# Kernel optimization log

Hardware: AMD Instinct MI355X
Metric: run time of the kernel (lower is better)

The kernel has to match this reference:

```python
import jax, jax.numpy as jnp
import numpy as np
import math

SEQLEN, DIM, N_HEADS = 2048, 4096, 32
HEAD_DIM = DIM // N_HEADS
NEG_INF = -1e30  # exp underflows to exactly 0, same effect as -inf without NaN risk


def setup_inputs() -> dict:
    key = jax.random.key(0)
    ks = jax.random.split(key, 7)
    scale = 1.0 / math.sqrt(DIM)
    x = jax.random.normal(ks[0], (SEQLEN, DIM), dtype=jnp.float32)
    weight_q = jax.random.normal(ks[1], (DIM, DIM), dtype=jnp.float32) * scale
    weight_k = jax.random.normal(ks[2], (DIM, DIM), dtype=jnp.float32) * scale
    weight_v = jax.random.normal(ks[3], (DIM, DIM), dtype=jnp.float32) * scale
    weight_o = jax.random.normal(ks[4], (DIM, DIM), dtype=jnp.float32) * scale
    # RoPE frequencies: freqs_cis = exp(i * t * theta_j), standard LLaMA schedule
    inv_freq = 1.0 / (10000.0 ** (np.arange(0, HEAD_DIM, 2, dtype=np.float32) / HEAD_DIM))
    angles = np.arange(SEQLEN, dtype=np.float32)[:, None] * inv_freq[None, :]  # [S, hd/2]
    freqs_cos = jnp.asarray(np.cos(angles), dtype=jnp.float32)
    freqs_sin = jnp.asarray(np.sin(angles), dtype=jnp.float32)
    # additive causal mask [S, S]
    mask = jnp.where(jnp.triu(jnp.ones((SEQLEN, SEQLEN), dtype=bool), k=1), NEG_INF, 0.0).astype(jnp.float32)
    return {"x": x, "weight_q": weight_q, "weight_k": weight_k, "weight_v": weight_v,
            "weight_o": weight_o, "freqs_cos": freqs_cos, "freqs_sin": freqs_sin,
            "mask": mask, "start_pos": 0}


def _apply_rope(t, cos, sin):
    # t: [S, H, hd]; cos/sin: [S, hd/2]
    tr = t.reshape(*t.shape[:-1], -1, 2)           # [S, H, hd/2, 2]
    t_re, t_im = tr[..., 0], tr[..., 1]
    c = cos[:, None, :]
    s = sin[:, None, :]
    out_re = t_re * c - t_im * s
    out_im = t_re * s + t_im * c
    return jnp.stack([out_re, out_im], axis=-1).reshape(t.shape)


def reference(x, weight_q, weight_k, weight_v, weight_o, freqs_cos, freqs_sin, mask, start_pos):
    S, D = x.shape
    hd = freqs_cos.shape[-1] * 2
    H = D // hd
    # the per-head double loop over wq[j][i] is exactly a full [D,D] projection
    xq = (x @ weight_q).reshape(S, H, hd)
    xk = (x @ weight_k).reshape(S, H, hd)
    xv = (x @ weight_v).reshape(S, H, hd)
    xq = _apply_rope(xq, freqs_cos, freqs_sin)
    xk = _apply_rope(xk, freqs_cos, freqs_sin)
    # start_pos == 0 prefill: cache slice == freshly computed keys/values
    scores = jnp.einsum('shd,thd->hst', xq, xk) / jnp.sqrt(jnp.float32(hd))
    scores = scores + mask[None, :, :]
    probs = jax.nn.softmax(scores.astype(jnp.float32), axis=-1).astype(xq.dtype)
    qkv = jnp.einsum('hst,thd->shd', probs, xv).reshape(S, D)
    return qkv @ weight_o
```

## Files before the change

### kernel.cpp

```cpp
#include <hip/hip_runtime.h>
#include <hip/hip_bf16.h>
#include <type_traits>

typedef __hip_bfloat16 bf16;
typedef __attribute__((ext_vector_type(8))) short s8v;
typedef __attribute__((ext_vector_type(4))) short s4v;
typedef __attribute__((ext_vector_type(4))) float f4v;

#define MFMA16(A, B, C) __builtin_amdgcn_mfma_f32_16x16x32_bf16((A), (B), (C), 0, 0, 0)

constexpr int SEQ = 2048;
constexpr int DIM = 4096;
constexpr int NH  = 32;
constexpr int HD  = 128;

__device__ __forceinline__ short f2bs(float f) {
    __hip_bfloat16_raw r = __float2bfloat16(f);
    return (short)r.x;
}

__device__ __forceinline__ void ld_g2l(const bf16* g, bf16* l) {
    __builtin_amdgcn_global_load_lds(
        (const __attribute__((address_space(1))) void*)g,
        (__attribute__((address_space(3))) void*)l, 16, 0, 0);
}

__global__ void convert_bf16(const float* __restrict__ s, bf16* __restrict__ d) {
    int i = blockIdx.x * blockDim.x + threadIdx.x;
    float4 f = ((const float4*)s)[i];
    s4v o;
    o[0] = f2bs(f.x); o[1] = f2bs(f.y); o[2] = f2bs(f.z); o[3] = f2bs(f.w);
    *(s4v*)(d + (size_t)i * 4) = o;
}

__global__ void convt_bf16(const float* __restrict__ src, bf16* __restrict__ dst,
                           int R, int C) {
    __shared__ float t[32][33];
    int c0 = blockIdx.x * 32, r0 = blockIdx.y * 32;
    int tx = threadIdx.x, ty = threadIdx.y;
#pragma unroll
    for (int i = 0; i < 4; i++)
        t[ty + 8 * i][tx] = src[(size_t)(r0 + ty + 8 * i) * C + c0 + tx];
    __syncthreads();
#pragma unroll
    for (int i = 0; i < 4; i++)
        dst[(size_t)(c0 + ty + 8 * i) * R + r0 + tx] = __float2bfloat16(t[tx][ty + 8 * i]);
}

template <typename CT>
__global__ __launch_bounds__(512, 2) void gemm_8p(const bf16* __restrict__ A,
                                                  const bf16* __restrict__ Bt,
                                                  CT* __restrict__ C,
                                                  int M, int N, int K) {
    __shared__ bf16 As_[2][128 * 64];
    __shared__ bf16 Bs_[2][256 * 64];
    const int tid  = threadIdx.x;
    const int lane = tid & 63;
    const int wv   = tid >> 6;
    const int m16  = lane & 15;
    const int quad = lane >> 4;
    const int wm   = wv >> 2, wn = wv & 3;
    const int bm   = blockIdx.y, bn = blockIdx.x;

    const bf16* Ab = A  + (size_t)bm * 128 * K;
    const bf16* Bb = Bt + (size_t)bn * 256 * K;

    const int i0   = wv * 64 + lane;
    const int row0 = i0 >> 3;
    const int gc8  = ((i0 & 7) ^ (row0 & 7)) * 8;
    const int dst0 = (wv * 64) * 8;
    const int dst1 = (512 + wv * 64) * 8;

    const int aB = (wm * 64 + m16) * 64;
    const int bB = (wn * 64 + m16) * 64;
    const int swz = m16 & 7;
    const int c0k = ((0 + quad) ^ swz) * 8;
    const int c1k = ((4 + quad) ^ swz) * 8;

    const int NT = K >> 6;

    f4v acc[4][4] = {};
    s8v aR[4][2], bR[4][2];

#define STAGEU(gb, lb) do { \
        ld_g2l((gb) + (size_t)row0 * K + gc8, (lb) + dst0); \
        ld_g2l((gb) + (size_t)(row0 + 64) * K + gc8, (lb) + dst1); } while (0)
#define LDA_(i, ks) aR[i][ks] = *(const s8v*)(Ac + aB + (i) * 1024 + ((ks) ? c1k : c0k))
#define LDB_(j, ks) bR[j][ks] = *(const s8v*)(Bc + bB + (j) * 1024 + ((ks) ? c1k : c0k))
#define MMQ(i, j) do { acc[i][j] = MFMA16(aR[i][0], bR[j][0], acc[i][j]); \
                       acc[i][j] = MFMA16(aR[i][1], bR[j][1], acc[i][j]); } while (0)
#define BARX()  __builtin_amdgcn_s_barrier()
#define LGKM0() do { asm volatile("s_waitcnt lgkmcnt(0)" ::: "memory"); \
                     __builtin_amdgcn_sched_barrier(0); } while (0)

    STAGEU(Ab, As_[0]);
    STAGEU(Bb, Bs_[0]);
    STAGEU(Bb + (size_t)128 * K, Bs_[0] + 128 * 64);
    if (NT > 1) {
        STAGEU(Bb + 64, Bs_[1]);
        STAGEU(Bb + (size_t)128 * K + 64, Bs_[1] + 128 * 64);
        STAGEU(Ab + 64, As_[1]);
        asm volatile("s_waitcnt vmcnt(6)" ::: "memory");
    } else {
        asm volatile("s_waitcnt vmcnt(0)" ::: "memory");
    }
    __builtin_amdgcn_sched_barrier(0);
    BARX();

    for (int t = 0; t < NT; ++t) {
        const int cur = t & 1;
        const bf16* Ac = As_[cur];
        const bf16* Bc = Bs_[cur];
        const bool more = (t + 2 < NT);
        const int k2 = (t + 2) << 6;

        LDA_(0, 0); LDA_(0, 1); LDA_(1, 0); LDA_(1, 1);
        LDB_(0, 0); LDB_(0, 1); LDB_(1, 0); LDB_(1, 1);
        BARX(); LGKM0();
        __builtin_amdgcn_s_setprio(1);
        MMQ(0, 0); MMQ(0, 1); MMQ(1, 0); MMQ(1, 1);
        __builtin_amdgcn_s_setprio(0);
        BARX();

        LDB_(2, 0); LDB_(2, 1); LDB_(3, 0); LDB_(3, 1);
        BARX(); LGKM0();
        __builtin_amdgcn_s_setprio(1);
        MMQ(0, 2); MMQ(0, 3); MMQ(1, 2); MMQ(1, 3);
        __builtin_amdgcn_s_setprio(0);
        BARX();

        LDA_(2, 0); LDA_(2, 1); LDA_(3, 0); LDA_(3, 1);
        if (more) {
            STAGEU(Bb + k2, Bs_[cur]);
            STAGEU(Bb + (size_t)128 * K + k2, Bs_[cur] + 128 * 64);
        }
        BARX(); LGKM0();
        __builtin_amdgcn_s_setprio(1);
        MMQ(2, 0); MMQ(2, 1); MMQ(3, 0); MMQ(3, 1);
        __builtin_amdgcn_s_setprio(0);
        BARX();

        if (more) {
            STAGEU(Ab + k2, As_[cur]);
            asm volatile("s_waitcnt vmcnt(6)" ::: "memory");
        } else {
            asm volatile("s_waitcnt vmcnt(0)" ::: "memory");
        }
        __builtin_amdgcn_sched_barrier(0);
        BARX();
        __builtin_amdgcn_s_setprio(1);
        MMQ(2, 2); MMQ(2, 3); MMQ(3, 2); MMQ(3, 3);
        __builtin_amdgcn_s_setprio(0);
        BARX();
    }

#undef STAGEU
#undef LDA_
#undef LDB_
#undef MMQ
#undef BARX
#undef LGKM0

#pragma unroll
    for (int i = 0; i < 4; i++)
#pragma unroll
        for (int j = 0; j < 4; j++)
#pragma unroll
            for (int r = 0; r < 4; r++) {
                int row = bm * 128 + wm * 64 + i * 16 + quad * 4 + r;
                int col = bn * 256 + wn * 64 + j * 16 + m16;
                if constexpr (std::is_same<CT, float>::value)
                    C[(size_t)row * N + col] = acc[i][j][r];
                else
                    C[(size_t)row * N + col] = __float2bfloat16(acc[i][j][r]);
            }
}

template <typename AT, typename CT>
__global__ __launch_bounds__(256) void gemm_nat(const AT* __restrict__ A,
                                                const float* __restrict__ B,
                                                CT* __restrict__ C,
                                                int M, int N, int K) {
    __shared__ short As[128][40];
    __shared__ short Bs[128][40];
    const int tid  = threadIdx.x;
    const int lane = tid & 63;
    const int w    = tid >> 6;
    const int m16  = lane & 15;
    const int quad = lane >> 4;
    const int wm   = w >> 1, wn = w & 1;
    const int bm   = blockIdx.y, bn = blockIdx.x;

    const AT* Ab = A + (size_t)bm * 128 * K;

    f4v acc[4][4] = {};
    const int r0 = tid >> 2;
    const int kc = (tid & 3) * 8;

    for (int k0 = 0; k0 < K; k0 += 32) {
        if constexpr (std::is_same<AT, float>::value) {
#pragma unroll
            for (int half = 0; half < 2; half++) {
                const float* src = Ab + (size_t)(r0 + 64 * half) * K + k0 + kc;
                float4 f0 = *(const float4*)(src);
                float4 f1 = *(const float4*)(src + 4);
                s8v t;
                t[0] = f2bs(f0.x); t[1] = f2bs(f0.y); t[2] = f2bs(f0.z); t[3] = f2bs(f0.w);
                t[4] = f2bs(f1.x); t[5] = f2bs(f1.y); t[6] = f2bs(f1.z); t[7] = f2bs(f1.w);
                *(s8v*)&As[r0 + 64 * half][kc] = t;
            }
        } else {
            *(s8v*)&As[r0][kc]      = *(const s8v*)(Ab + (size_t)r0 * K + k0 + kc);
            *(s8v*)&As[r0 + 64][kc] = *(const s8v*)(Ab + (size_t)(r0 + 64) * K + k0 + kc);
        }
#pragma unroll
        for (int v = tid; v < 512; v += 256) {
            int kr = v >> 4;
            int nc = (v & 15) * 8;
            const float* src = B + (size_t)(k0 + kr) * N + bn * 128 + nc;
            float4 f0 = *(const float4*)(src);
            float4 f1 = *(const float4*)(src + 4);
            Bs[nc + 0][kr] = f2bs(f0.x); Bs[nc + 1][kr] = f2bs(f0.y);
            Bs[nc + 2][kr] = f2bs(f0.z); Bs[nc + 3][kr] = f2bs(f0.w);
            Bs[nc + 4][kr] = f2bs(f1.x); Bs[nc + 5][kr] = f2bs(f1.y);
            Bs[nc + 6][kr] = f2bs(f1.z); Bs[nc + 7][kr] = f2bs(f1.w);
        }
        __syncthreads();

        s8v a[4], b[4];
#pragma unroll
        for (int i = 0; i < 4; i++) a[i] = *(s8v*)&As[wm * 64 + i * 16 + m16][quad * 8];
#pragma unroll
        for (int j = 0; j < 4; j++) b[j] = *(s8v*)&Bs[wn * 64 + j * 16 + m16][quad * 8];
#pragma unroll
        for (int i = 0; i < 4; i++)
#pragma unroll
            for (int j = 0; j < 4; j++) acc[i][j] = MFMA16(a[i], b[j], acc[i][j]);
        __syncthreads();
    }

#pragma unroll
    for (int i = 0; i < 4; i++)
#pragma unroll
        for (int j = 0; j < 4; j++)
#pragma unroll
            for (int r = 0; r < 4; r++) {
                int row = bm * 128 + wm * 64 + i * 16 + quad * 4 + r;
                int col = bn * 128 + wn * 64 + j * 16 + m16;
                if constexpr (std::is_same<CT, float>::value)
                    C[(size_t)row * N + col] = acc[i][j][r];
                else
                    C[(size_t)row * N + col] = __float2bfloat16(acc[i][j][r]);
            }
}

__global__ void rope_kernel(bf16* __restrict__ Q, bf16* __restrict__ K,
                            const float* __restrict__ fc, const float* __restrict__ fs) {
    int tid = blockIdx.x * blockDim.x + threadIdx.x;
    int s = tid >> 11;
    int r = tid & 2047;
    int i = r & 63;
    float c  = fc[s * 64 + i];
    float sn = fs[s * 64 + i];
    size_t idx = (size_t)s * DIM + 2 * r;
    float qre = __bfloat162float(Q[idx]), qim = __bfloat162float(Q[idx + 1]);
    Q[idx]     = __float2bfloat16(qre * c - qim * sn);
    Q[idx + 1] = __float2bfloat16(qre * sn + qim * c);
    float kre = __bfloat162float(K[idx]), kim = __bfloat162float(K[idx + 1]);
    K[idx]     = __float2bfloat16(kre * c - kim * sn);
    K[idx + 1] = __float2bfloat16(kre * sn + kim * c);
}

__global__ __launch_bounds__(256) void attn_kernel(const bf16* __restrict__ Q,
                                                   const bf16* __restrict__ K,
                                                   const bf16* __restrict__ V,
                                                   bf16* __restrict__ O) {
    __shared__ short Ks[64][136];
    __shared__ short Vs[128][72];
    __shared__ short Ps[64][72];

    const int qb = (int)gridDim.x - 1 - (int)blockIdx.x;
    const int h  = blockIdx.y;
    const int tid  = threadIdx.x;
    const int w    = tid >> 6;
    const int lane = tid & 63;
    const int m16  = lane & 15;
    const int quad = lane >> 4;
    const float scale = 0.08838834764831845f;

    const int rn  = tid >> 4;
    const int rc  = (tid & 15) * 8;
    const int dcs = (tid & 15) & 7;

    s8v aq[4];
    {
        const bf16* qp = Q + (size_t)(qb * 64 + w * 16 + m16) * DIM + h * HD + quad * 8;
#pragma unroll
        for (int ks = 0; ks < 4; ks++) aq[ks] = *(const s8v*)(qp + ks * 32);
    }

    f4v acc[8] = {};
    float mrow[4] = {-1e30f, -1e30f, -1e30f, -1e30f};
    float lrow[4] = {};

    s8v kreg[4], vreg[4];
    {
        const bf16* kp = K + (size_t)rn * DIM + h * HD + rc;
        const bf16* vp = V + (size_t)rn * DIM + h * HD + rc;
#pragma unroll
        for (int it = 0; it < 4; it++) {
            kreg[it] = *(const s8v*)(kp + (size_t)it * 16 * DIM);
            vreg[it] = *(const s8v*)(vp + (size_t)it * 16 * DIM);
        }
    }

    for (int kt = 0; kt <= qb; kt++) {
#pragma unroll
        for (int it = 0; it < 4; it++)
            *(s8v*)&Ks[it * 16 + rn][rc] = kreg[it];
#pragma unroll
        for (int it = 0; it < 4; it++) {
            int n   = it * 16 + rn;
            int col = (((n >> 3) ^ dcs) << 3) | (n & 7);
#pragma unroll
            for (int e = 0; e < 8; e++) Vs[rc + e][col] = vreg[it][e];
        }
        __syncthreads();

        if (kt < qb) {
            const bf16* kp = K + (size_t)((kt + 1) * 64 + rn) * DIM + h * HD + rc;
            const bf16* vp = V + (size_t)((kt + 1) * 64 + rn) * DIM + h * HD + rc;
#pragma unroll
            for (int it = 0; it < 4; it++) {
                kreg[it] = *(const s8v*)(kp + (size_t)it * 16 * DIM);
                vreg[it] = *(const s8v*)(vp + (size_t)it * 16 * DIM);
            }
        }

        f4v sc[4] = {};
#pragma unroll
        for (int j = 0; j < 4; j++)
#pragma unroll
            for (int ks = 0; ks < 4; ks++) {
                s8v bk = *(s8v*)&Ks[j * 16 + m16][ks * 32 + quad * 8];
                sc[j] = MFMA16(aq[ks], bk, sc[j]);
            }

        const bool diag = (kt == qb);
#pragma unroll
        for (int j = 0; j < 4; j++)
#pragma unroll
            for (int r = 0; r < 4; r++) {
                float sv = sc[j][r] * scale;
                if (diag && (j * 16 + m16) > (w * 16 + quad * 4 + r)) sv = -1e30f;
                sc[j][r] = sv;
            }

#pragma unroll
        for (int r = 0; r < 4; r++) {
            float mx = fmaxf(fmaxf(sc[0][r], sc[1][r]), fmaxf(sc[2][r], sc[3][r]));
#pragma unroll
            for (int off = 1; off < 16; off <<= 1) mx = fmaxf(mx, __shfl_xor(mx, off, 64));
            float mn    = fmaxf(mrow[r], mx);
            float alpha = __expf(mrow[r] - mn);
            mrow[r] = mn;
            float rs = 0.f;
#pragma unroll
            for (int j = 0; j < 4; j++) {
                float p = __expf(sc[j][r] - mn);
                sc[j][r] = p;
                rs += p;
            }
#pragma unroll
            for (int off = 1; off < 16; off <<= 1) rs += __shfl_xor(rs, off, 64);
            lrow[r] = lrow[r] * alpha + rs;
#pragma unroll
            for (int jo = 0; jo < 8; jo++) acc[jo][r] = acc[jo][r] * alpha;
        }

#pragma unroll
        for (int j = 0; j < 4; j++)
#pragma unroll
            for (int r = 0; r < 4; r++)
                Ps[w * 16 + quad * 4 + r][j * 16 + m16] = f2bs(sc[j][r]);
        asm volatile("s_waitcnt lgkmcnt(0)" ::: "memory");
        __builtin_amdgcn_sched_barrier(0);

#pragma unroll
        for (int ks2 = 0; ks2 < 2; ks2++) {
            s8v ap = *(s8v*)&Ps[w * 16 + m16][ks2 * 32 + quad * 8];
#pragma unroll
            for (int jo = 0; jo < 8; jo++) {
                int dv = jo * 16 + m16;
                int cg = (((ks2 * 4 + quad) ^ ((dv >> 3) & 7)) << 3);
                s8v bv = *(s8v*)&Vs[dv][cg];
                acc[jo] = MFMA16(ap, bv, acc[jo]);
            }
        }
        __syncthreads();
    }

#pragma unroll
    for (int jo = 0; jo < 8; jo++)
#pragma unroll
        for (int r = 0; r < 4; r++) {
            float o = acc[jo][r] / fmaxf(lrow[r], 1e-30f);
            int row = qb * 64 + w * 16 + quad * 4 + r;
            int col = h * HD + jo * 16 + m16;
            O[(size_t)row * DIM + col] = __float2bfloat16(o);
        }
}

extern "C" void kernel_launch(void* const* d_in, const int* in_sizes, int n_in,
                              void* d_out, int out_size, void* d_ws, size_t ws_size,
                              hipStream_t stream) {
    const float* x  = (const float*)d_in[0];
    const float* wq = (const float*)d_in[1];
    const float* wk = (const float*)d_in[2];
    const float* wv = (const float*)d_in[3];
    const float* wo = (const float*)d_in[4];
    const float* fc = (const float*)d_in[5];
    const float* fs = (const float*)d_in[6];

    float* out = (float*)d_out;

    const size_t SZ = (size_t)SEQ * DIM;
    const size_t WZ = (size_t)DIM * DIM;
    bf16* Q  = (bf16*)d_ws;
    bf16* Kb = Q + SZ;
    bf16* V  = Kb + SZ;
    bf16* AO = V + SZ;

    const size_t need = (5 * SZ + WZ) * sizeof(bf16);

    if (ws_size >= need) {
        bf16* xb = AO + SZ;
        bf16* wb = xb + SZ;

        dim3 tB(32, 8), tGw(DIM / 32, DIM / 32);
        dim3 gG8(DIM / 256, SEQ / 128);

        convert_bf16<<<(int)(SZ / 4 / 256), 256, 0, stream>>>(x, xb);

        convt_bf16<<<tGw, tB, 0, stream>>>(wq, wb, DIM, DIM);
        gemm_8p<bf16><<<gG8, 512, 0, stream>>>(xb, wb, Q, SEQ, DIM, DIM);
        convt_bf16<<<tGw, tB, 0, stream>>>(wk, wb, DIM, DIM);
        gemm_8p<bf16><<<gG8, 512, 0, stream>>>(xb, wb, Kb, SEQ, DIM, DIM);
        convt_bf16<<<tGw, tB, 0, stream>>>(wv, wb, DIM, DIM);
        gemm_8p<bf16><<<gG8, 512, 0, stream>>>(xb, wb, V, SEQ, DIM, DIM);

        rope_kernel<<<(SEQ * (DIM / 2)) / 256, 256, 0, stream>>>(Q, Kb, fc, fs);
        attn_kernel<<<dim3(SEQ / 64, NH), 256, 0, stream>>>(Q, Kb, V, AO);

        convt_bf16<<<tGw, tB, 0, stream>>>(wo, wb, DIM, DIM);
        gemm_8p<float><<<gG8, 512, 0, stream>>>(AO, wb, out, SEQ, DIM, DIM);
    } else {
        dim3 gGn(DIM / 128, SEQ / 128);
        gemm_nat<float, bf16><<<gGn, 256, 0, stream>>>(x, wq, Q,  SEQ, DIM, DIM);
        gemm_nat<float, bf16><<<gGn, 256, 0, stream>>>(x, wk, Kb, SEQ, DIM, DIM);
        gemm_nat<float, bf16><<<gGn, 256, 0, stream>>>(x, wv, V,  SEQ, DIM, DIM);
        rope_kernel<<<(SEQ * (DIM / 2)) / 256, 256, 0, stream>>>(Q, Kb, fc, fs);
        attn_kernel<<<dim3(SEQ / 64, NH), 256, 0, stream>>>(Q, Kb, V, AO);
        gemm_nat<bf16, float><<<gGn, 256, 0, stream>>>(AO, wo, out, SEQ, DIM, DIM);
    }
}
```

Before: 836.8 us.

## Pair causal attention query blocks, vectorize weight transpose, remap GEMM block order

Each attention block now processes two query tiles, p and NQB-1-p, so every workgroup does the same amount of causal work, and the grid is halved. The fp32-to-bf16 weight transpose now uses 64x64 tiles with float4 loads and 16-byte bf16 stores. The GEMM also remaps its block index so that consecutive blocks share B column tiles, which should improve L2 reuse. The GEMM remap hardcodes the grid shape (16 column blocks by 16 row blocks), and halving the attention grid lowers the number of blocks available to fill the GPU.

```diff
diff --git a/kernel.cpp b/kernel.cpp
--- a/kernel.cpp
+++ b/kernel.cpp
@@ -33,18 +33,32 @@
     *(s4v*)(d + (size_t)i * 4) = o;
 }
 
-__global__ void convt_bf16(const float* __restrict__ src, bf16* __restrict__ dst,
-                           int R, int C) {
-    __shared__ float t[32][33];
-    int c0 = blockIdx.x * 32, r0 = blockIdx.y * 32;
-    int tx = threadIdx.x, ty = threadIdx.y;
-#pragma unroll
-    for (int i = 0; i < 4; i++)
-        t[ty + 8 * i][tx] = src[(size_t)(r0 + ty + 8 * i) * C + c0 + tx];
+__global__ __launch_bounds__(256) void convt_bf16(const float* __restrict__ src,
+                                                  bf16* __restrict__ dst,
+                                                  int R, int C) {
+    __shared__ float t[64][65];
+    const int c0 = blockIdx.x * 64, r0 = blockIdx.y * 64;
+    const int tid = threadIdx.x;
+    const int lr = tid >> 4;
+    const int lc = (tid & 15) * 4;
+#pragma unroll
+    for (int i = 0; i < 4; i++) {
+        float4 f = *(const float4*)(src + (size_t)(r0 + lr + 16 * i) * C + c0 + lc);
+        t[lr + 16 * i][lc]     = f.x;
+        t[lr + 16 * i][lc + 1] = f.y;
+        t[lr + 16 * i][lc + 2] = f.z;
+        t[lr + 16 * i][lc + 3] = f.w;
+    }
     __syncthreads();
-#pragma unroll
-    for (int i = 0; i < 4; i++)
-        dst[(size_t)(c0 + ty + 8 * i) * R + r0 + tx] = __float2bfloat16(t[tx][ty + 8 * i]);
+    const int oc = tid >> 2;
+#pragma unroll
+    for (int i = 0; i < 2; i++) {
+        int rr = (tid & 3) * 8 + 32 * i;
+        s8v o;
+#pragma unroll
+        for (int e = 0; e < 8; e++) o[e] = f2bs(t[rr + e][oc]);
+        *(s8v*)(dst + (size_t)(c0 + oc) * R + r0 + rr) = o;
+    }
 }
 
 template <typename CT>
@@ -60,7 +74,11 @@
     const int m16  = lane & 15;
     const int quad = lane >> 4;
     const int wm   = wv >> 2, wn = wv & 3;
-    const int bm   = blockIdx.y, bn = blockIdx.x;
+
+    const int v   = (int)(blockIdx.y * gridDim.x + blockIdx.x);
+    const int s_  = v >> 3;
+    const int bn  = (v & 7) * 2 + (s_ >> 4);
+    const int bm  = s_ & 15;
 
     const bf16* Ab = A  + (size_t)bm * 128 * K;
     const bf16* Bb = Bt + (size_t)bn * 256 * K;
@@ -279,7 +297,7 @@
     __shared__ short Vs[128][72];
     __shared__ short Ps[64][72];
 
-    const int qb = (int)gridDim.x - 1 - (int)blockIdx.x;
+    const int p  = blockIdx.x;
     const int h  = blockIdx.y;
     const int tid  = threadIdx.x;
     const int w    = tid >> 6;
@@ -287,49 +305,30 @@
     const int m16  = lane & 15;
     const int quad = lane >> 4;
     const float scale = 0.08838834764831845f;
+    const int NQB = (int)gridDim.x * 2;
 
     const int rn  = tid >> 4;
     const int rc  = (tid & 15) * 8;
     const int dcs = (tid & 15) & 7;
 
-    s8v aq[4];
-    {
-        const bf16* qp = Q + (size_t)(qb * 64 + w * 16 + m16) * DIM + h * HD + quad * 8;
-#pragma unroll
-        for (int ks = 0; ks < 4; ks++) aq[ks] = *(const s8v*)(qp + ks * 32);
-    }
-
-    f4v acc[8] = {};
-    float mrow[4] = {-1e30f, -1e30f, -1e30f, -1e30f};
-    float lrow[4] = {};
-
-    s8v kreg[4], vreg[4];
-    {
-        const bf16* kp = K + (size_t)rn * DIM + h * HD + rc;
-        const bf16* vp = V + (size_t)rn * DIM + h * HD + rc;
-#pragma unroll
-        for (int it = 0; it < 4; it++) {
-            kreg[it] = *(const s8v*)(kp + (size_t)it * 16 * DIM);
-            vreg[it] = *(const s8v*)(vp + (size_t)it * 16 * DIM);
-        }
-    }
-
-    for (int kt = 0; kt <= qb; kt++) {
-#pragma unroll
-        for (int it = 0; it < 4; it++)
-            *(s8v*)&Ks[it * 16 + rn][rc] = kreg[it];
-#pragma unroll
-        for (int it = 0; it < 4; it++) {
-            int n   = it * 16 + rn;
-            int col = (((n >> 3) ^ dcs) << 3) | (n & 7);
-#pragma unroll
-            for (int e = 0; e < 8; e++) Vs[rc + e][col] = vreg[it][e];
-        }
-        __syncthreads();
-
-        if (kt < qb) {
-            const bf16* kp = K + (size_t)((kt + 1) * 64 + rn) * DIM + h * HD + rc;
-            const bf16* vp = V + (size_t)((kt + 1) * 64 + rn) * DIM + h * HD + rc;
+    for (int half = 0; half < 2; half++) {
+        const int qb = half ? (NQB - 1 - p) : p;
+
+        s8v aq[4];
+        {
+            const bf16* qp = Q + (size_t)(qb * 64 + w * 16 + m16) * DIM + h * HD + quad * 8;
+#pragma unroll
+            for (int ks = 0; ks < 4; ks++) aq[ks] = *(const s8v*)(qp + ks * 32);
+        }
+
+        f4v acc[8] = {};
+        float mrow[4] = {-1e30f, -1e30f, -1e30f, -1e30f};
+        float lrow[4] = {};
+
+        s8v kreg[4], vreg[4];
+        {
+            const bf16* kp = K + (size_t)rn * DIM + h * HD + rc;
+            const bf16* vp = V + (size_t)rn * DIM + h * HD + rc;
 #pragma unroll
             for (int it = 0; it < 4; it++) {
                 kreg[it] = *(const s8v*)(kp + (size_t)it * 16 * DIM);
@@ -337,78 +336,102 @@
             }
         }
 
-        f4v sc[4] = {};
-#pragma unroll
-        for (int j = 0; j < 4; j++)
-#pragma unroll
-            for (int ks = 0; ks < 4; ks++) {
-                s8v bk = *(s8v*)&Ks[j * 16 + m16][ks * 32 + quad * 8];
-                sc[j] = MFMA16(aq[ks], bk, sc[j]);
-            }
-
-        const bool diag = (kt == qb);
-#pragma unroll
-        for (int j = 0; j < 4; j++)
+        for (int kt = 0; kt <= qb; kt++) {
+#pragma unroll
+            for (int it = 0; it < 4; it++)
+                *(s8v*)&Ks[it * 16 + rn][rc] = kreg[it];
+#pragma unroll
+            for (int it = 0; it < 4; it++) {
+                int n   = it * 16 + rn;
+                int col = (((n >> 3) ^ dcs) << 3) | (n & 7);
+#pragma unroll
+                for (int e = 0; e < 8; e++) Vs[rc + e][col] = vreg[it][e];
+            }
+            __syncthreads();
+
+            if (kt < qb) {
+                const bf16* kp = K + (size_t)((kt + 1) * 64 + rn) * DIM + h * HD + rc;
+                const bf16* vp = V + (size_t)((kt + 1) * 64 + rn) * DIM + h * HD + rc;
+#pragma unroll
+                for (int it = 0; it < 4; it++) {
+                    kreg[it] = *(const s8v*)(kp + (size_t)it * 16 * DIM);
+                    vreg[it] = *(const s8v*)(vp + (size_t)it * 16 * DIM);
+                }
+            }
+
+            f4v sc[4] = {};
+#pragma unroll
+            for (int j = 0; j < 4; j++)
+#pragma unroll
+                for (int ks = 0; ks < 4; ks++) {
+                    s8v bk = *(s8v*)&Ks[j * 16 + m16][ks * 32 + quad * 8];
+                    sc[j] = MFMA16(aq[ks], bk, sc[j]);
+                }
+
+            const bool diag = (kt == qb);
+#pragma unroll
+            for (int j = 0; j < 4; j++)
+#pragma unroll
+                for (int r = 0; r < 4; r++) {
+                    float sv = sc[j][r] * scale;
+                    if (diag && (j * 16 + m16) > (w * 16 + quad * 4 + r)) sv = -1e30f;
+                    sc[j][r] = sv;
+                }
+
 #pragma unroll
             for (int r = 0; r < 4; r++) {
-                float sv = sc[j][r] * scale;
-                if (diag && (j * 16 + m16) > (w * 16 + quad * 4 + r)) sv = -1e30f;
-                sc[j][r] = sv;
-            }
-
-#pragma unroll
-        for (int r = 0; r < 4; r++) {
-            float mx = fmaxf(fmaxf(sc[0][r], sc[1][r]), fmaxf(sc[2][r], sc[3][r]));
-#pragma unroll
-            for (int off = 1; off < 16; off <<= 1) mx = fmaxf(mx, __shfl_xor(mx, off, 64));
-            float mn    = fmaxf(mrow[r], mx);
-            float alpha = __expf(mrow[r] - mn);
-            mrow[r] = mn;
-            float rs = 0.f;
-#pragma unroll
-            for (int j = 0; j < 4; j++) {
-                float p = __expf(sc[j][r] - mn);
-                sc[j][r] = p;
-                rs += p;
-            }
-#pragma unroll
-            for (int off = 1; off < 16; off <<= 1) rs += __shfl_xor(rs, off, 64);
-            lrow[r] = lrow[r] * alpha + rs;
-#pragma unroll
-            for (int jo = 0; jo < 8; jo++) acc[jo][r] = acc[jo][r] * alpha;
-        }
-
-#pragma unroll
-        for (int j = 0; j < 4; j++)
-#pragma unroll
-            for (int r = 0; r < 4; r++)
-                Ps[w * 16 + quad * 4 + r][j * 16 + m16] = f2bs(sc[j][r]);
-        asm volatile("s_waitcnt lgkmcnt(0)" ::: "memory");
-        __builtin_amdgcn_sched_barrier(0);
-
-#pragma unroll
-        for (int ks2 = 0; ks2 < 2; ks2++) {
-            s8v ap = *(s8v*)&Ps[w * 16 + m16][ks2 * 32 + quad * 8];
-#pragma unroll
-            for (int jo = 0; jo < 8; jo++) {
-                int dv = jo * 16 + m16;
-                int cg = (((ks2 * 4 + quad) ^ ((dv >> 3) & 7)) << 3);
-                s8v bv = *(s8v*)&Vs[dv][cg];
-                acc[jo] = MFMA16(ap, bv, acc[jo]);
-            }
-        }
-        __syncthreads();
-    }
-
-#pragma unroll
-    for (int jo = 0; jo < 8; jo++)
-#pragma unroll
-        for (int r = 0; r < 4; r++) {
-            float o = acc[jo][r] / fmaxf(lrow[r], 1e-30f);
-            int row = qb * 64 + w * 16 + quad * 4 + r;
-            int col = h * HD + jo * 16 + m16;
-            O[(size_t)row * DIM + col] = __float2bfloat16(o);
-        }
+                float mx = fmaxf(fmaxf(sc[0][r], sc[1][r]), fmaxf(sc[2][r], sc[3][r]));
+#pragma unroll
+                for (int off = 1; off < 16; off <<= 1) mx = fmaxf(mx, __shfl_xor(mx, off, 64));
+                float mn    = fmaxf(mrow[r], mx);
+                float alpha = __expf(mrow[r] - mn);
+                mrow[r] = mn;
+                float rs = 0.f;
+#pragma unroll
+                for (int j = 0; j < 4; j++) {
+                    float pj = __expf(sc[j][r] - mn);
+                    sc[j][r] = pj;
+                    rs += pj;
+                }
+#pragma unroll
+                for (int off = 1; off < 16; off <<= 1) rs += __shfl_xor(rs, off, 64);
+                lrow[r] = lrow[r] * alpha + rs;
+#pragma unroll
+                for (int jo = 0; jo < 8; jo++) acc[jo][r] = acc[jo][r] * alpha;
+            }
+
+#pragma unroll
+            for (int j = 0; j < 4; j++)
+#pragma unroll
+                for (int r = 0; r < 4; r++)
+                    Ps[w * 16 + quad * 4 + r][j * 16 + m16] = f2bs(sc[j][r]);
+            asm volatile("s_waitcnt lgkmcnt(0)" ::: "memory");
+            __builtin_amdgcn_sched_barrier(0);
+
+#pragma unroll
+            for (int ks2 = 0; ks2 < 2; ks2++) {
+                s8v ap = *(s8v*)&Ps[w * 16 + m16][ks2 * 32 + quad * 8];
+#pragma unroll
+                for (int jo = 0; jo < 8; jo++) {
+                    int dv = jo * 16 + m16;
+                    int cg = (((ks2 * 4 + quad) ^ ((dv >> 3) & 7)) << 3);
+                    s8v bv = *(s8v*)&Vs[dv][cg];
+                    acc[jo] = MFMA16(ap, bv, acc[jo]);
+                }
+            }
+            __syncthreads();
+        }
+
+#pragma unroll
+        for (int jo = 0; jo < 8; jo++)
+#pragma unroll
+            for (int r = 0; r < 4; r++) {
+                float o = acc[jo][r] / fmaxf(lrow[r], 1e-30f);
+                int row = qb * 64 + w * 16 + quad * 4 + r;
+                int col = h * HD + jo * 16 + m16;
+                O[(size_t)row * DIM + col] = __float2bfloat16(o);
+            }
+    }
 }
 
 extern "C" void kernel_launch(void* const* d_in, const int* in_sizes, int n_in,
@@ -437,22 +460,22 @@
         bf16* xb = AO + SZ;
         bf16* wb = xb + SZ;
 
-        dim3 tB(32, 8), tGw(DIM / 32, DIM / 32);
+        dim3 tGw(DIM / 64, DIM / 64);
         dim3 gG8(DIM / 256, SEQ / 128);
 
         convert_bf16<<<(int)(SZ / 4 / 256), 256, 0, stream>>>(x, xb);
 
-        convt_bf16<<<tGw, tB, 0, stream>>>(wq, wb, DIM, DIM);
+        convt_bf16<<<tGw, 256, 0, stream>>>(wq, wb, DIM, DIM);
         gemm_8p<bf16><<<gG8, 512, 0, stream>>>(xb, wb, Q, SEQ, DIM, DIM);
-        convt_bf16<<<tGw, tB, 0, stream>>>(wk, wb, DIM, DIM);
+        convt_bf16<<<tGw, 256, 0, stream>>>(wk, wb, DIM, DIM);
         gemm_8p<bf16><<<gG8, 512, 0, stream>>>(xb, wb, Kb, SEQ, DIM, DIM);
-        convt_bf16<<<tGw, tB, 0, stream>>>(wv, wb, DIM, DIM);
+        convt_bf16<<<tGw, 256, 0, stream>>>(wv, wb, DIM, DIM);
         gemm_8p<bf16><<<gG8, 512, 0, stream>>>(xb, wb, V, SEQ, DIM, DIM);
 
         rope_kernel<<<(SEQ * (DIM / 2)) / 256, 256, 0, stream>>>(Q, Kb, fc, fs);
-        attn_kernel<<<dim3(SEQ / 64, NH), 256, 0, stream>>>(Q, Kb, V, AO);
-
-        convt_bf16<<<tGw, tB, 0, stream>>>(wo, wb, DIM, DIM);
+        attn_kernel<<<dim3(SEQ / 128, NH), 256, 0, stream>>>(Q, Kb, V, AO);
+
+        convt_bf16<<<tGw, 256, 0, stream>>>(wo, wb, DIM, DIM);
         gemm_8p<float><<<gG8, 512, 0, stream>>>(AO, wb, out, SEQ, DIM, DIM);
     } else {
         dim3 gGn(DIM / 128, SEQ / 128);
@@ -460,7 +483,7 @@
         gemm_nat<float, bf16><<<gGn, 256, 0, stream>>>(x, wk, Kb, SEQ, DIM, DIM);
         gemm_nat<float, bf16><<<gGn, 256, 0, stream>>>(x, wv, V,  SEQ, DIM, DIM);
         rope_kernel<<<(SEQ * (DIM / 2)) / 256, 256, 0, stream>>>(Q, Kb, fc, fs);
-        attn_kernel<<<dim3(SEQ / 64, NH), 256, 0, stream>>>(Q, Kb, V, AO);
+        attn_kernel<<<dim3(SEQ / 128, NH), 256, 0, stream>>>(Q, Kb, V, AO);
         gemm_nat<bf16, float><<<gGn, 256, 0, stream>>>(AO, wo, out, SEQ, DIM, DIM);
     }
 }
```

New measurement: 752.9 us. 10.0% less time.
